# Performance work log

Measured on AMD Instinct MI355X. Metric: run time of the kernel, lower is better.

The kernel has to match this reference:

```python
import jax, jax.numpy as jnp
import numpy as np

V = 1.0e10           # large init value for non-seed pixels (FastGeodis v)
LAMB = 0.0           # lamb=0 => pure Euclidean raster-scan distance
ITERS = 2            # FastGeodis iterations
THRESH = 0.7         # binarize_map threshold
TOPO_WEIGHT = 0.005
TOPO_WINDOW = 64
EPS = 1e-6
BIG = 1e20


def _sweep_down(dist, image):
    # One top-down raster sweep of the FastGeodis up-down pass.
    # dist, image: [H, W]. Row r updates from row r-1 at col offsets {-1,0,+1}
    # with squared spatial distances {2,1,2}; lamb weights the intensity term.
    W = dist.shape[1]
    sp2 = (2.0, 1.0, 2.0)

    def step(carry, xs):
        pd, pi = carry          # previous-row distance / intensity, [W]
        d_row, i_row = xs
        pd_pad = jnp.pad(pd, 1, constant_values=BIG)
        pi_pad = jnp.pad(pi, 1, constant_values=0.0)
        new = d_row
        for k in range(3):
            p = pd_pad[k:k + W]
            q = i_row - pi_pad[k:k + W]
            new = jnp.minimum(new, p + jnp.sqrt(sp2[k] + LAMB * q * q))
        return (new, i_row), new

    (_, _), rest = jax.lax.scan(step, (dist[0], image[0]), (dist[1:], image[1:]))
    return jnp.concatenate([dist[:1], rest], axis=0)


def _updown(dist, image):
    dist = _sweep_down(dist, image)
    dist = _sweep_down(dist[::-1], image[::-1])[::-1]
    return dist


def generalised_geodesic2d(image, softmask):
    # image: intensity map [H,W]; softmask: [H,W]; dist init = V * softmask.
    dist = V * softmask
    for _ in range(ITERS):
        dist = _updown(dist, image)
        dist = _updown(dist.T, image.T).T
    return dist


def calculate_edt(inp):
    # Original: softmask = inp, intensity image = 1 - inp (mask_pt = 1 - image_pt).
    return generalised_geodesic2d(1.0 - inp, inp)


def _global_norm(x):
    return (x - x.min()) / (x.max() - x.min() + EPS)


def _topo_loss(p, t, window):
    # Persistence-style matching proxy: within each non-overlapping window,
    # match level-set values of pred and target by sorting (0-dim persistence
    # birth/death values of the filtration are order statistics of the window)
    # and penalize squared differences of matched values.
    H, W = p.shape
    nh, nw = H // window, W // window

    def win_sort(x):
        x = x.reshape(nh, window, nw, window).transpose(0, 2, 1, 3)
        return jnp.sort(x.reshape(nh * nw, window * window), axis=-1)

    return jnp.mean((win_sort(p) - win_sort(t)) ** 2)


def _per_item(pred_i, target_i):
    # pred_i/target_i: [C, H, W]; pred already remapped to [0, 1]
    bin_pred = (pred_i >= THRESH).astype(jnp.float32)
    comb_pred = jnp.max(bin_pred, axis=0)        # combine_channels
    comb_tgt = jnp.max(target_i, axis=0)
    edt_p = _global_norm(calculate_edt(1.0 - comb_pred))
    edt_t = _global_norm(calculate_edt(1.0 - comb_tgt))
    return _topo_loss(edt_p, edt_t, TOPO_WINDOW)


def setup_inputs():
    key = jax.random.key(0)
    k1, k2 = jax.random.split(key)
    B, C, H, W = 16, 3, 512, 512
    pred = jax.random.normal(k1, (B, C, H, W), dtype=jnp.float32)  # model output in ~[-1,1]
    # target: binary multi-channel cell masks (sparse foreground)
    target = (jax.random.uniform(k2, (B, C, H, W)) > 0.8).astype(jnp.float32)
    return {"pred": pred, "target": target}


def reference(pred, target):
    pred01 = (pred + 1.0) / 2.0
    losses = jax.vmap(_per_item)(pred01.astype(jnp.float32), target.astype(jnp.float32))
    mean_loss = losses.mean()
    return (mean_loss * TOPO_WEIGHT, mean_loss)
```

## Files before the change

kernel.cpp:

```cpp
#include <hip/hip_runtime.h>

#define BIGF 1e20f
#define VF   1e10f

constexpr float SQ2 = 1.41421356237309515f;

__device__ __forceinline__ float dpp_left(float x)
{
    int o = __builtin_amdgcn_update_dpp(0x60AD78ECu , __float_as_int(x),
                                        0x138, 0xF, 0xF, false);
    return __int_as_float(o);
}
__device__ __forceinline__ float dpp_right(float x)
{
    int o = __builtin_amdgcn_update_dpp(0x60AD78ECu , __float_as_int(x),
                                        0x130, 0xF, 0xF, false);
    return __int_as_float(o);
}

__device__ __forceinline__ void load_row8(const float* __restrict__ M, int r, int c0, float v[8])
{
    const float4* q = (const float4*)(M + ((long)r << 9) + c0);
    float4 a = q[0], b = q[1];
    v[0] = a.x; v[1] = a.y; v[2] = a.z; v[3] = a.w;
    v[4] = b.x; v[5] = b.y; v[6] = b.z; v[7] = b.w;
}
__device__ __forceinline__ void store_row8(float* __restrict__ M, int r, int c0, const float v[8])
{
    float4* q = (float4*)(M + ((long)r << 9) + c0);
    q[0] = make_float4(v[0], v[1], v[2], v[3]);
    q[1] = make_float4(v[4], v[5], v[6], v[7]);
}

__device__ __forceinline__ void step8(const float cur[8], const float p[8], float nv[8])
{
    float left  = dpp_left(p[7]);
    float right = dpp_right(p[0]);
    #pragma unroll
    for (int j = 0; j < 8; ++j) {
        float l  = (j == 0) ? left  : p[j - 1];
        float rr = (j == 7) ? right : p[j + 1];
        nv[j] = fminf(fminf(cur[j], p[j] + 1.0f), fminf(l, rr) + SQ2);
    }
}

__global__ __launch_bounds__(256) void k_init(const float* __restrict__ pred,
                                              const float* __restrict__ tgt,
                                              float* __restrict__ bufA,
                                              float* __restrict__ acc,
                                              unsigned* __restrict__ count,
                                              float* __restrict__ minmax)
{
    if (blockIdx.x == 0 && threadIdx.x == 0) { *acc = 0.0f; *count = 0u; }
    if (blockIdx.x == 0 && threadIdx.x < 64)
        minmax[threadIdx.x] = (threadIdx.x & 1) ? 0.0f : BIGF;

    int r = blockIdx.x & 7;
    int k = blockIdx.x >> 3;
    int b = r + 8 * (k >> 10);
    int pix = (k & 1023) * 256 + threadIdx.x;
    long base = (long)b * 3 * 262144 + pix;

    float p0 = pred[base], p1 = pred[base + 262144], p2 = pred[base + 2 * 262144];
    bool fgP = ((p0 + 1.0f) * 0.5f >= 0.7f) ||
               ((p1 + 1.0f) * 0.5f >= 0.7f) ||
               ((p2 + 1.0f) * 0.5f >= 0.7f);

    float t0 = tgt[base], t1 = tgt[base + 262144], t2 = tgt[base + 2 * 262144];
    float mt = fmaxf(fmaxf(t0, t1), t2);

    bufA[(long)b * 262144 + pix]        = fgP ? 0.0f : VF;
    bufA[(long)(16 + b) * 262144 + pix] = VF * (1.0f - mt);
}

__global__ __launch_bounds__(64) void k_p1d(const float* __restrict__ X0,
                                            float* __restrict__ Cb)
{
    int bi = blockIdx.x, m = bi >> 4, w = bi & 15;
    const float* X = X0 + ((long)m << 18);
    int c0 = (int)threadIdx.x << 3, a = w << 5;
    float p[8]; load_row8(X, a, c0, p);
    float buf[4][8];
    #pragma unroll
    for (int k = 1; k <= 3; ++k) load_row8(X, a + k, c0, buf[k & 3]);
    #pragma unroll
    for (int i = 1; i < 32; ++i) {
        if (i + 3 < 32) load_row8(X, a + i + 3, c0, buf[(i + 3) & 3]);
        float nv[8]; step8(buf[i & 3], p, nv);
        #pragma unroll
        for (int j = 0; j < 8; ++j) p[j] = nv[j];
    }
    float4* o = (float4*)(Cb + m * 8192 + w * 512 + c0);
    o[0] = make_float4(p[0], p[1], p[2], p[3]);
    o[1] = make_float4(p[4], p[5], p[6], p[7]);
}

__device__ __forceinline__ void combine(float* __restrict__ bwp, float* __restrict__ part,
                                        int wdst, int wsrc, int t, int wave, int lane,
                                        const float wreg[8])
{
    const float* bs = bwp + wsrc * 576;
    if (wave <= 8) {
        int base = lane * 8 + 8 * wave;
        float W[16];
        float4 W0 = *(const float4*)(bs + base);
        float4 W1 = *(const float4*)(bs + base + 4);
        W[0]=W0.x; W[1]=W0.y; W[2]=W0.z; W[3]=W0.w;
        W[4]=W1.x; W[5]=W1.y; W[6]=W1.z; W[7]=W1.w;
        float acc[8];
        if (wave < 8) {
            float4 W2 = *(const float4*)(bs + base + 8);
            float4 W3 = *(const float4*)(bs + base + 12);
            W[8]=W2.x; W[9]=W2.y; W[10]=W2.z; W[11]=W2.w;
            W[12]=W3.x; W[13]=W3.y; W[14]=W3.z; W[15]=W3.w;
            #pragma unroll
            for (int j = 0; j < 8; ++j) acc[j] = W[j] + wreg[0];
            #pragma unroll
            for (int dt = 1; dt < 8; ++dt)
                #pragma unroll
                for (int j = 0; j < 8; ++j)
                    acc[j] = fminf(acc[j], W[j + dt] + wreg[dt]);
        } else {
            #pragma unroll
            for (int j = 0; j < 8; ++j) acc[j] = W[j] + wreg[0];
        }
        float4* pp = (float4*)(part + wave * 512 + lane * 8);
        pp[0] = make_float4(acc[0], acc[1], acc[2], acc[3]);
        pp[1] = make_float4(acc[4], acc[5], acc[6], acc[7]);
    }
    __syncthreads();
    if (t < 512) {
        float r = bwp[wdst * 576 + 32 + t];
        #pragma unroll
        for (int p2 = 0; p2 < 9; ++p2) r = fminf(r, part[p2 * 512 + t]);
        bwp[wdst * 576 + 32 + t] = r;
    }
    __syncthreads();
}

__global__ __launch_bounds__(1024) void k_comb(float* __restrict__ Cb, int dir)
{
    __shared__ __align__(16) float bwp[16 * 576];
    __shared__ __align__(16) float part[9 * 512];
    __shared__ float wgt[72];
    int m = blockIdx.x, t = threadIdx.x, wave = t >> 6, lane = t & 63, c0 = lane << 3;
    float* Cm = Cb + m * 8192;

    bwp[wave * 576 + ((lane < 32) ? lane : lane + 512)] = BIGF;
    *(float4*)(bwp + wave * 576 + 32 + c0)     = *(const float4*)(Cm + wave * 512 + c0);
    *(float4*)(bwp + wave * 576 + 32 + c0 + 4) = *(const float4*)(Cm + wave * 512 + c0 + 4);
    if (t < 65) { int d = t - 32; int ad = d < 0 ? -d : d; wgt[t] = ad * SQ2 + (float)(32 - ad); }
    __syncthreads();
    float wreg[8];
    #pragma unroll
    for (int dt = 0; dt < 8; ++dt) wreg[dt] = BIGF;
    if (wave < 8) {
        #pragma unroll
        for (int dt = 0; dt < 8; ++dt) wreg[dt] = wgt[wave * 8 + dt];
    } else if (wave == 8) wreg[0] = wgt[64];

    #pragma unroll 1
    for (int i = 0; i < 15; ++i) {
        int w2 = (dir > 0) ? (1 + i) : (14 - i);
        combine(bwp, part, w2, w2 - dir, t, wave, lane, wreg);
    }
    *(float4*)(Cm + wave * 512 + c0)     = *(const float4*)(bwp + wave * 576 + 32 + c0);
    *(float4*)(Cm + wave * 512 + c0 + 4) = *(const float4*)(bwp + wave * 576 + 32 + c0 + 4);
}

__global__ __launch_bounds__(64) void k_p3d1u(const float* __restrict__ X0,
                                              float* __restrict__ Y0,
                                              const float* __restrict__ Cb,
                                              float* __restrict__ Db)
{
    int bi = blockIdx.x, m = bi >> 4, w = bi & 15;
    const float* X = X0 + ((long)m << 18);
    float* Y = Y0 + ((long)m << 18);
    int c0 = (int)threadIdx.x << 3, a = w << 5;
    float p[8], buf[4][8];

    if (w == 0) {
        load_row8(X, 0, c0, p);
        store_row8(Y, 0, c0, p);
        #pragma unroll
        for (int k = 1; k <= 3; ++k) load_row8(X, k, c0, buf[k & 3]);
        #pragma unroll
        for (int i = 1; i < 32; ++i) {
            if (i + 3 < 32) load_row8(X, i + 3, c0, buf[(i + 3) & 3]);
            float nv[8]; step8(buf[i & 3], p, nv);
            store_row8(Y, i, c0, nv);
            #pragma unroll
            for (int j = 0; j < 8; ++j) p[j] = nv[j];
        }
    } else {
        const float4* s = (const float4*)(Cb + m * 8192 + (w - 1) * 512 + c0);
        float4 s0 = s[0], s1 = s[1];
        p[0]=s0.x; p[1]=s0.y; p[2]=s0.z; p[3]=s0.w;
        p[4]=s1.x; p[5]=s1.y; p[6]=s1.z; p[7]=s1.w;
        #pragma unroll
        for (int k = 0; k < 3; ++k) load_row8(X, a + k, c0, buf[k & 3]);
        #pragma unroll
        for (int i = 0; i < 32; ++i) {
            if (i + 3 < 32) load_row8(X, a + i + 3, c0, buf[(i + 3) & 3]);
            float nv[8]; step8(buf[i & 3], p, nv);
            store_row8(Y, a + i, c0, nv);
            #pragma unroll
            for (int j = 0; j < 8; ++j) p[j] = nv[j];
        }
    }

    float q[8];
    #pragma unroll
    for (int j = 0; j < 8; ++j) q[j] = p[j];
    #pragma unroll
    for (int k = 1; k <= 3; ++k) load_row8(Y, a + 31 - k, c0, buf[k & 3]);
    #pragma unroll
    for (int i = 1; i < 32; ++i) {
        if (i + 3 < 32) load_row8(Y, a + 31 - (i + 3), c0, buf[(i + 3) & 3]);
        float nv[8]; step8(buf[i & 3], q, nv);
        #pragma unroll
        for (int j = 0; j < 8; ++j) q[j] = nv[j];
    }
    float4* o = (float4*)(Db + m * 8192 + w * 512 + c0);
    o[0] = make_float4(q[0], q[1], q[2], q[3]);
    o[1] = make_float4(q[4], q[5], q[6], q[7]);
}

__device__ __forceinline__ void tile_store(float* tile, int h, int c0, const float v[8])
{
    float4* q = (float4*)(tile + h * 516 + c0);
    q[0] = make_float4(v[0], v[1], v[2], v[3]);
    q[1] = make_float4(v[4], v[5], v[6], v[7]);
}
__device__ __forceinline__ void half_out(const float* tile, float* __restrict__ Xo,
                                         int a2, int L)
{
    int g = L >> 2, j = (L & 3) << 2;
    #pragma unroll
    for (int it = 0; it < 32; ++it) {
        int c = (it << 4) + g;
        float4 v = make_float4(tile[(j + 0) * 516 + c], tile[(j + 1) * 516 + c],
                               tile[(j + 2) * 516 + c], tile[(j + 3) * 516 + c]);
        *(float4*)(Xo + (long)c * 512 + a2 + j) = v;
    }
}

__global__ __launch_bounds__(64) void k_p3u(const float* __restrict__ Y0,
                                            float* __restrict__ Xo0,
                                            const float* __restrict__ Db,
                                            float* __restrict__ minmax,
                                            int final_pass)
{
    __shared__ __align__(16) float tile[16 * 516];
    int bi = blockIdx.x, m = bi >> 4, w = bi & 15;
    const float* Y = Y0 + ((long)m << 18);
    float* Xo = Xo0 + ((long)m << 18);
    int L = threadIdx.x, c0 = L << 3, a = w << 5;
    float p[8], buf[4][8];
    float mn = BIGF, mx = -BIGF;

    if (w == 15) {
        load_row8(Y, 511, c0, p);
        tile_store(tile, 15, c0, p);
        #pragma unroll
        for (int j = 0; j < 8; ++j) { mn = fminf(mn, p[j]); mx = fmaxf(mx, p[j]); }
        #pragma unroll
        for (int k = 1; k <= 3; ++k) load_row8(Y, 511 - k, c0, buf[k & 3]);
        #pragma unroll
        for (int i = 1; i < 16; ++i) {
            load_row8(Y, 511 - (i + 3), c0, buf[(i + 3) & 3]);
            float nv[8]; step8(buf[i & 3], p, nv);
            tile_store(tile, 15 - i, c0, nv);
            #pragma unroll
            for (int j = 0; j < 8; ++j) { p[j] = nv[j]; mn = fminf(mn, nv[j]); mx = fmaxf(mx, nv[j]); }
        }
        half_out(tile, Xo, a + 16, L);
        #pragma unroll
        for (int i = 16; i < 32; ++i) {
            if (i + 3 < 32) load_row8(Y, 511 - (i + 3), c0, buf[(i + 3) & 3]);
            float nv[8]; step8(buf[i & 3], p, nv);
            tile_store(tile, 31 - i, c0, nv);
            #pragma unroll
            for (int j = 0; j < 8; ++j) { p[j] = nv[j]; mn = fminf(mn, nv[j]); mx = fmaxf(mx, nv[j]); }
        }
        half_out(tile, Xo, a, L);
    } else {
        const float4* s = (const float4*)(Db + m * 8192 + (w + 1) * 512 + c0);
        float4 s0 = s[0], s1 = s[1];
        p[0]=s0.x; p[1]=s0.y; p[2]=s0.z; p[3]=s0.w;
        p[4]=s1.x; p[5]=s1.y; p[6]=s1.z; p[7]=s1.w;
        #pragma unroll
        for (int k = 0; k < 3; ++k) load_row8(Y, a + 31 - k, c0, buf[k & 3]);
        #pragma unroll
        for (int i = 0; i < 16; ++i) {
            load_row8(Y, a + 31 - (i + 3), c0, buf[(i + 3) & 3]);
            float nv[8]; step8(buf[i & 3], p, nv);
            tile_store(tile, 15 - i, c0, nv);
            #pragma unroll
            for (int j = 0; j < 8; ++j) { p[j] = nv[j]; mn = fminf(mn, nv[j]); mx = fmaxf(mx, nv[j]); }
        }
        half_out(tile, Xo, a + 16, L);
        #pragma unroll
        for (int i = 16; i < 32; ++i) {
            if (i + 3 < 32) load_row8(Y, a + 31 - (i + 3), c0, buf[(i + 3) & 3]);
            float nv[8]; step8(buf[i & 3], p, nv);
            tile_store(tile, 31 - i, c0, nv);
            #pragma unroll
            for (int j = 0; j < 8; ++j) { p[j] = nv[j]; mn = fminf(mn, nv[j]); mx = fmaxf(mx, nv[j]); }
        }
        half_out(tile, Xo, a, L);
    }

    if (final_pass) {
        for (int o = 32; o > 0; o >>= 1) {
            mn = fminf(mn, __shfl_down(mn, o));
            mx = fmaxf(mx, __shfl_down(mx, o));
        }
        if (L == 0) {
            atomicMin((int*)(minmax + 2 * m),     __float_as_int(mn));
            atomicMax((int*)(minmax + 2 * m + 1), __float_as_int(mx));
        }
    }
}

__device__ __forceinline__ void ce(float& a, float& b, bool up)
{
    float lo = fminf(a, b), hi = fmaxf(a, b);
    a = up ? lo : hi;
    b = up ? hi : lo;
}
__device__ __forceinline__ void merge8(float v[8], bool up)
{
    ce(v[0], v[4], up); ce(v[1], v[5], up); ce(v[2], v[6], up); ce(v[3], v[7], up);
    ce(v[0], v[2], up); ce(v[1], v[3], up); ce(v[4], v[6], up); ce(v[5], v[7], up);
    ce(v[0], v[1], up); ce(v[2], v[3], up); ce(v[4], v[5], up); ce(v[6], v[7], up);
}
__device__ __forceinline__ void sort8(float v[8], bool u8)
{
    ce(v[0], v[1], true);  ce(v[2], v[3], false);
    ce(v[4], v[5], true);  ce(v[6], v[7], false);
    ce(v[0], v[2], true);  ce(v[1], v[3], true);
    ce(v[4], v[6], false); ce(v[5], v[7], false);
    ce(v[0], v[1], true);  ce(v[2], v[3], true);
    ce(v[4], v[5], false); ce(v[6], v[7], false);
    merge8(v, u8);
}
__device__ __forceinline__ void xstage(float v[8], int j8, bool keepmin)
{
    #pragma unroll
    for (int e = 0; e < 8; ++e) {
        float o = __shfl_xor(v[e], j8);
        v[e] = keepmin ? fminf(v[e], o) : fmaxf(v[e], o);
    }
}
__device__ __forceinline__ void lstage2(float p[8], float q[8], int j8, bool keepmin,
                                        float* sp, float* st, int t)
{
    __syncthreads();
    float4* wp = (float4*)(sp + t * 8);
    float4* wq = (float4*)(st + t * 8);
    wp[0] = make_float4(p[0], p[1], p[2], p[3]);
    wp[1] = make_float4(p[4], p[5], p[6], p[7]);
    wq[0] = make_float4(q[0], q[1], q[2], q[3]);
    wq[1] = make_float4(q[4], q[5], q[6], q[7]);
    __syncthreads();
    int pt = t ^ j8;
    const float4* rp = (const float4*)(sp + pt * 8);
    const float4* rq = (const float4*)(st + pt * 8);
    float4 a = rp[0], bb = rp[1], c = rq[0], d = rq[1];
    float op[8] = {a.x, a.y, a.z, a.w, bb.x, bb.y, bb.z, bb.w};
    float oq[8] = {c.x, c.y, c.z, c.w, d.x, d.y, d.z, d.w};
    #pragma unroll
    for (int e = 0; e < 8; ++e) {
        p[e] = keepmin ? fminf(p[e], op[e]) : fmaxf(p[e], op[e]);
        q[e] = keepmin ? fminf(q[e], oq[e]) : fmaxf(q[e], oq[e]);
    }
}

__global__ __launch_bounds__(512) void k_loss(const float* __restrict__ bufB,
                                              const float* __restrict__ minmax,
                                              float* __restrict__ acc,
                                              unsigned* __restrict__ count,
                                              float* __restrict__ out)
{
    __shared__ float sp[4096];
    __shared__ float st[4096];
    __shared__ float rs[8];

    int t = threadIdx.x;
    int r = blockIdx.x & 7;
    int k = blockIdx.x >> 3;
    int b = r + 8 * (k >> 6);
    int w = k & 63;
    int wi = w >> 3, wj = w & 7;

    int i0 = t << 3;
    int y = wi * 64 + (i0 >> 6);
    int x = wj * 64 + (i0 & 63);

    float mnP = minmax[2 * b],        mxP = minmax[2 * b + 1];
    float mnT = minmax[2 * (16 + b)], mxT = minmax[2 * (16 + b) + 1];
    float sclP = 1.0f / (mxP - mnP + 1e-6f);
    float sclT = 1.0f / (mxT - mnT + 1e-6f);

    float p[8], q[8];
    {
        const float4* P4 = (const float4*)(bufB + (long)b * 262144 + y * 512 + x);
        const float4* T4 = (const float4*)(bufB + (long)(16 + b) * 262144 + y * 512 + x);
        float4 a = P4[0], bb = P4[1], c = T4[0], d = T4[1];
        p[0]=a.x; p[1]=a.y; p[2]=a.z; p[3]=a.w; p[4]=bb.x; p[5]=bb.y; p[6]=bb.z; p[7]=bb.w;
        q[0]=c.x; q[1]=c.y; q[2]=c.z; q[3]=c.w; q[4]=d.x;  q[5]=d.y;  q[6]=d.z;  q[7]=d.w;
        #pragma unroll
        for (int e = 0; e < 8; ++e) {
            p[e] = (p[e] - mnP) * sclP;
            q[e] = (q[e] - mnT) * sclT;
        }
    }

    bool u8 = ((t & 1) == 0);
    sort8(p, u8);
    sort8(q, u8);

    for (int kk = 16; kk <= 4096; kk <<= 1) {
        bool u = ((i0 & kk) == 0);
        for (int j = kk >> 1; j >= 8; j >>= 1) {
            bool l = ((i0 & j) == 0);
            bool keepmin = (u == l);
            int j8 = j >> 3;
            if (j8 < 64) {
                xstage(p, j8, keepmin);
                xstage(q, j8, keepmin);
            } else {
                lstage2(p, q, j8, keepmin, sp, st, t);
            }
        }
        merge8(p, u);
        merge8(q, u);
    }

    float s = 0.0f;
    #pragma unroll
    for (int e = 0; e < 8; ++e) { float d = p[e] - q[e]; s += d * d; }
    for (int o = 32; o > 0; o >>= 1) s += __shfl_down(s, o);
    if ((t & 63) == 0) rs[t >> 6] = s;
    __syncthreads();
    if (t == 0) {
        float tot = 0.0f;
        #pragma unroll
        for (int i = 0; i < 8; ++i) tot += rs[i];
        atomicAdd(acc, tot);
        __threadfence();
        unsigned done = atomicAdd(count, 1u);
        if (done == 1023u) {
            float total = atomicAdd(acc, 0.0f);
            float mean = total * (1.0f / 4194304.0f);
            out[0] = mean * 0.005f;
            out[1] = mean;
        }
    }
}

extern "C" void kernel_launch(void* const* d_in, const int* in_sizes, int n_in,
                              void* d_out, int out_size, void* d_ws, size_t ws_size,
                              hipStream_t stream)
{
    const float* pred = (const float*)d_in[0];
    const float* tgt  = (const float*)d_in[1];
    float* out = (float*)d_out;

    char* ws = (char*)d_ws;
    float* bufA     = (float*)ws;
    float* bufB     = (float*)(ws + (32ull << 20));
    float* Cb       = (float*)(ws + (64ull << 20));
    float* Db       = (float*)(ws + (65ull << 20));
    float* minmax   = (float*)(ws + (66ull << 20));
    float* acc      = minmax + 64;
    unsigned* count = (unsigned*)(acc + 1);

    k_init<<<16 * 1024, 256, 0, stream>>>(pred, tgt, bufA, acc, count, minmax);

    for (int s = 0; s < 4; ++s) {
        k_p1d  <<<512,   64, 0, stream>>>(bufA, Cb);
        k_comb <<< 32, 1024, 0, stream>>>(Cb, +1);
        k_p3d1u<<<512,   64, 0, stream>>>(bufA, bufB, Cb, Db);
        k_comb <<< 32, 1024, 0, stream>>>(Db, -1);
        k_p3u  <<<512,   64, 0, stream>>>(bufB, bufA, Db, minmax, s == 3 ? 1 : 0);
    }

    k_loss<<<1024, 512, 0, stream>>>(bufA, minmax, acc, count, out);
}
```

Baseline: 457.4 us.

## Stash sweep rows in LDS and rewrite bitonic sort with med3 and DPP

The column-block kernel now keeps the 31 rows it just produced in shared memory, so the reverse sweep reads them from LDS instead of re-reading global memory. The loss kernel's bitonic sort becomes an all-ascending variant that uses reversed partner exchanges. Compare-exchanges become fmed3 against a plus or minus infinity selector, and the small-stride exchanges use DPP quad permutes instead of shuffles. This removes direction branches and cuts cross-lane traffic, but adds 62KB of LDS per block in the sweep kernel, which may limit occupancy.

```diff
diff --git a/kernel.cpp b/kernel.cpp
--- a/kernel.cpp
+++ b/kernel.cpp
@@ -16,6 +16,16 @@
     int o = __builtin_amdgcn_update_dpp(0x60AD78ECu , __float_as_int(x),
                                         0x130, 0xF, 0xF, false);
     return __int_as_float(o);
+}
+template<int CTRL>
+__device__ __forceinline__ float qdpp(float x)
+{
+    return __int_as_float(__builtin_amdgcn_update_dpp(0, __float_as_int(x),
+                                                      CTRL, 0xF, 0xF, true));
+}
+__device__ __forceinline__ float fmed3(float a, float b, float c)
+{
+    return __builtin_amdgcn_fmed3f(a, b, c);
 }
 
 __device__ __forceinline__ void load_row8(const float* __restrict__ M, int r, int c0, float v[8])
@@ -173,15 +183,19 @@
                                               const float* __restrict__ Cb,
                                               float* __restrict__ Db)
 {
+    __shared__ __align__(16) float stash[31 * 512];
     int bi = blockIdx.x, m = bi >> 4, w = bi & 15;
     const float* X = X0 + ((long)m << 18);
     float* Y = Y0 + ((long)m << 18);
-    int c0 = (int)threadIdx.x << 3, a = w << 5;
+    const int L = threadIdx.x;
+    int c0 = L << 3, a = w << 5;
     float p[8], buf[4][8];
 
     if (w == 0) {
         load_row8(X, 0, c0, p);
         store_row8(Y, 0, c0, p);
+        *(float4*)(stash + 0 * 512 + L * 4)       = make_float4(p[0], p[1], p[2], p[3]);
+        *(float4*)(stash + 0 * 512 + 256 + L * 4) = make_float4(p[4], p[5], p[6], p[7]);
         #pragma unroll
         for (int k = 1; k <= 3; ++k) load_row8(X, k, c0, buf[k & 3]);
         #pragma unroll
@@ -189,6 +203,10 @@
             if (i + 3 < 32) load_row8(X, i + 3, c0, buf[(i + 3) & 3]);
             float nv[8]; step8(buf[i & 3], p, nv);
             store_row8(Y, i, c0, nv);
+            if (i < 31) {
+                *(float4*)(stash + i * 512 + L * 4)       = make_float4(nv[0], nv[1], nv[2], nv[3]);
+                *(float4*)(stash + i * 512 + 256 + L * 4) = make_float4(nv[4], nv[5], nv[6], nv[7]);
+            }
             #pragma unroll
             for (int j = 0; j < 8; ++j) p[j] = nv[j];
         }
@@ -204,22 +222,40 @@
             if (i + 3 < 32) load_row8(X, a + i + 3, c0, buf[(i + 3) & 3]);
             float nv[8]; step8(buf[i & 3], p, nv);
             store_row8(Y, a + i, c0, nv);
+            if (i < 31) {
+                *(float4*)(stash + i * 512 + L * 4)       = make_float4(nv[0], nv[1], nv[2], nv[3]);
+                *(float4*)(stash + i * 512 + 256 + L * 4) = make_float4(nv[4], nv[5], nv[6], nv[7]);
+            }
             #pragma unroll
             for (int j = 0; j < 8; ++j) p[j] = nv[j];
         }
     }
 
-    float q[8];
+    float q[8], cur[8];
     #pragma unroll
     for (int j = 0; j < 8; ++j) q[j] = p[j];
-    #pragma unroll
-    for (int k = 1; k <= 3; ++k) load_row8(Y, a + 31 - k, c0, buf[k & 3]);
+    {
+        float4 x0 = *(const float4*)(stash + 30 * 512 + L * 4);
+        float4 x1 = *(const float4*)(stash + 30 * 512 + 256 + L * 4);
+        cur[0]=x0.x; cur[1]=x0.y; cur[2]=x0.z; cur[3]=x0.w;
+        cur[4]=x1.x; cur[5]=x1.y; cur[6]=x1.z; cur[7]=x1.w;
+    }
     #pragma unroll
     for (int i = 1; i < 32; ++i) {
-        if (i + 3 < 32) load_row8(Y, a + 31 - (i + 3), c0, buf[(i + 3) & 3]);
-        float nv[8]; step8(buf[i & 3], q, nv);
+        float nxt[8];
+        if (i < 31) {
+            float4 x0 = *(const float4*)(stash + (30 - i) * 512 + L * 4);
+            float4 x1 = *(const float4*)(stash + (30 - i) * 512 + 256 + L * 4);
+            nxt[0]=x0.x; nxt[1]=x0.y; nxt[2]=x0.z; nxt[3]=x0.w;
+            nxt[4]=x1.x; nxt[5]=x1.y; nxt[6]=x1.z; nxt[7]=x1.w;
+        }
+        float nv[8]; step8(cur, q, nv);
         #pragma unroll
         for (int j = 0; j < 8; ++j) q[j] = nv[j];
+        if (i < 31) {
+            #pragma unroll
+            for (int j = 0; j < 8; ++j) cur[j] = nxt[j];
+        }
     }
     float4* o = (float4*)(Db + m * 8192 + w * 512 + c0);
     o[0] = make_float4(q[0], q[1], q[2], q[3]);
@@ -323,38 +359,63 @@
     }
 }
 
-__device__ __forceinline__ void ce(float& a, float& b, bool up)
-{
-    float lo = fminf(a, b), hi = fmaxf(a, b);
-    a = up ? lo : hi;
-    b = up ? hi : lo;
-}
-__device__ __forceinline__ void merge8(float v[8], bool up)
-{
-    ce(v[0], v[4], up); ce(v[1], v[5], up); ce(v[2], v[6], up); ce(v[3], v[7], up);
-    ce(v[0], v[2], up); ce(v[1], v[3], up); ce(v[4], v[6], up); ce(v[5], v[7], up);
-    ce(v[0], v[1], up); ce(v[2], v[3], up); ce(v[4], v[5], up); ce(v[6], v[7], up);
-}
-__device__ __forceinline__ void sort8(float v[8], bool u8)
-{
-    ce(v[0], v[1], true);  ce(v[2], v[3], false);
-    ce(v[4], v[5], true);  ce(v[6], v[7], false);
-    ce(v[0], v[2], true);  ce(v[1], v[3], true);
-    ce(v[4], v[6], false); ce(v[5], v[7], false);
-    ce(v[0], v[1], true);  ce(v[2], v[3], true);
-    ce(v[4], v[5], false); ce(v[6], v[7], false);
-    merge8(v, u8);
-}
-__device__ __forceinline__ void xstage(float v[8], int j8, bool keepmin)
+__device__ __forceinline__ void cex(float& lo, float& hi)
+{
+    float l = fminf(lo, hi);
+    hi = fmaxf(lo, hi);
+    lo = l;
+}
+__device__ __forceinline__ void merge8asc(float v[8])
+{
+    cex(v[0],v[4]); cex(v[1],v[5]); cex(v[2],v[6]); cex(v[3],v[7]);
+    cex(v[0],v[2]); cex(v[1],v[3]); cex(v[4],v[6]); cex(v[5],v[7]);
+    cex(v[0],v[1]); cex(v[2],v[3]); cex(v[4],v[5]); cex(v[6],v[7]);
+}
+__device__ __forceinline__ void sort8asc(float v[8])
+{
+    cex(v[0],v[1]); cex(v[2],v[3]); cex(v[4],v[5]); cex(v[6],v[7]);
+    cex(v[0],v[3]); cex(v[1],v[2]); cex(v[4],v[7]); cex(v[5],v[6]);
+    cex(v[0],v[1]); cex(v[2],v[3]); cex(v[4],v[5]); cex(v[6],v[7]);
+    cex(v[0],v[7]); cex(v[1],v[6]); cex(v[2],v[5]); cex(v[3],v[4]);
+    cex(v[0],v[2]); cex(v[1],v[3]); cex(v[4],v[6]); cex(v[5],v[7]);
+    cex(v[0],v[1]); cex(v[2],v[3]); cex(v[4],v[5]); cex(v[6],v[7]);
+}
+__device__ __forceinline__ void xshfl(float v[8], int j8, float sel)
 {
     #pragma unroll
     for (int e = 0; e < 8; ++e) {
         float o = __shfl_xor(v[e], j8);
-        v[e] = keepmin ? fminf(v[e], o) : fmaxf(v[e], o);
-    }
-}
-__device__ __forceinline__ void lstage2(float p[8], float q[8], int j8, bool keepmin,
-                                        float* sp, float* st, int t)
+        v[e] = fmed3(v[e], o, sel);
+    }
+}
+template<int CTRL>
+__device__ __forceinline__ void xdpp(float v[8], float sel)
+{
+    #pragma unroll
+    for (int e = 0; e < 8; ++e) {
+        float o = qdpp<CTRL>(v[e]);
+        v[e] = fmed3(v[e], o, sel);
+    }
+}
+__device__ __forceinline__ void rshfl(float v[8], int tmask, float sel)
+{
+    float o[8];
+    #pragma unroll
+    for (int e = 0; e < 8; ++e) o[e] = __shfl_xor(v[7 - e], tmask);
+    #pragma unroll
+    for (int e = 0; e < 8; ++e) v[e] = fmed3(v[e], o[e], sel);
+}
+template<int CTRL>
+__device__ __forceinline__ void rdpp(float v[8], float sel)
+{
+    float o[8];
+    #pragma unroll
+    for (int e = 0; e < 8; ++e) o[e] = qdpp<CTRL>(v[7 - e]);
+    #pragma unroll
+    for (int e = 0; e < 8; ++e) v[e] = fmed3(v[e], o[e], sel);
+}
+__device__ __forceinline__ void lstage(float p[8], float q[8], int tmask, float sel, bool rev,
+                                       float* sp, float* st, int t)
 {
     __syncthreads();
     float4* wp = (float4*)(sp + t * 8);
@@ -364,16 +425,24 @@
     wq[0] = make_float4(q[0], q[1], q[2], q[3]);
     wq[1] = make_float4(q[4], q[5], q[6], q[7]);
     __syncthreads();
-    int pt = t ^ j8;
+    int pt = t ^ tmask;
     const float4* rp = (const float4*)(sp + pt * 8);
     const float4* rq = (const float4*)(st + pt * 8);
     float4 a = rp[0], bb = rp[1], c = rq[0], d = rq[1];
-    float op[8] = {a.x, a.y, a.z, a.w, bb.x, bb.y, bb.z, bb.w};
-    float oq[8] = {c.x, c.y, c.z, c.w, d.x, d.y, d.z, d.w};
-    #pragma unroll
-    for (int e = 0; e < 8; ++e) {
-        p[e] = keepmin ? fminf(p[e], op[e]) : fmaxf(p[e], op[e]);
-        q[e] = keepmin ? fminf(q[e], oq[e]) : fmaxf(q[e], oq[e]);
+    float op[8] = {a.x,a.y,a.z,a.w,bb.x,bb.y,bb.z,bb.w};
+    float oq[8] = {c.x,c.y,c.z,c.w,d.x,d.y,d.z,d.w};
+    if (rev) {
+        #pragma unroll
+        for (int e = 0; e < 8; ++e) {
+            p[e] = fmed3(p[e], op[7 - e], sel);
+            q[e] = fmed3(q[e], oq[7 - e], sel);
+        }
+    } else {
+        #pragma unroll
+        for (int e = 0; e < 8; ++e) {
+            p[e] = fmed3(p[e], op[e], sel);
+            q[e] = fmed3(q[e], oq[e], sel);
+        }
     }
 }
 
@@ -417,25 +486,28 @@
         }
     }
 
-    bool u8 = ((t & 1) == 0);
-    sort8(p, u8);
-    sort8(q, u8);
-
+    const float INFP = __builtin_inff();
+    sort8asc(p); sort8asc(q);
+
+    #pragma unroll 1
     for (int kk = 16; kk <= 4096; kk <<= 1) {
-        bool u = ((i0 & kk) == 0);
-        for (int j = kk >> 1; j >= 8; j >>= 1) {
-            bool l = ((i0 & j) == 0);
-            bool keepmin = (u == l);
+        int tmask = (kk - 1) >> 3;
+        float sel = ((t & (kk >> 4)) == 0) ? -INFP : INFP;
+        if (kk == 16)        { rdpp<0xB1>(p, sel); rdpp<0xB1>(q, sel); }
+        else if (kk == 32)   { rdpp<0x1B>(p, sel); rdpp<0x1B>(q, sel); }
+        else if (tmask < 64) { rshfl(p, tmask, sel); rshfl(q, tmask, sel); }
+        else                 lstage(p, q, tmask, sel, true, sp, st, t);
+
+        #pragma unroll 1
+        for (int j = kk >> 2; j >= 8; j >>= 1) {
             int j8 = j >> 3;
-            if (j8 < 64) {
-                xstage(p, j8, keepmin);
-                xstage(q, j8, keepmin);
-            } else {
-                lstage2(p, q, j8, keepmin, sp, st, t);
-            }
-        }
-        merge8(p, u);
-        merge8(q, u);
+            float s2 = ((t & j8) == 0) ? -INFP : INFP;
+            if (j8 == 1)      { xdpp<0xB1>(p, s2); xdpp<0xB1>(q, s2); }
+            else if (j8 == 2) { xdpp<0x4E>(p, s2); xdpp<0x4E>(q, s2); }
+            else if (j8 < 64) { xshfl(p, j8, s2); xshfl(q, j8, s2); }
+            else              lstage(p, q, j8, s2, false, sp, st, t);
+        }
+        merge8asc(p); merge8asc(q);
     }
 
     float s = 0.0f;
```

New measurement: 409.5 us. -10.5%, faster.
